# Optimization experiments

Measured on AMD Instinct MI355X. Metric: run time of the kernel, lower is better.

Reference implementation:

```python
import jax, jax.numpy as jnp
import numpy as np

NUM_INPUTS = 256
L1, L2 = 256, 128
NUM_ACTIONS = 17
NUM_EXPERTS = 4
GATE_H = 32
BATCH = 131072


def setup_inputs() -> dict:
    key = jax.random.key(0)
    ks = jax.random.split(key, 16)
    s = 0.05
    return {
        "x": jax.random.normal(ks[0], (BATCH, NUM_INPUTS), jnp.float32),
        # stacked expert weights [E, in, out]
        "W1": jax.random.normal(ks[1], (NUM_EXPERTS, NUM_INPUTS, L1), jnp.float32) * s,
        "b1": jax.random.normal(ks[2], (NUM_EXPERTS, L1), jnp.float32) * s,
        "W2": jax.random.normal(ks[3], (NUM_EXPERTS, L1, L2), jnp.float32) * s,
        "b2": jax.random.normal(ks[4], (NUM_EXPERTS, L2), jnp.float32) * s,
        "Wmu": jax.random.normal(ks[5], (NUM_EXPERTS, L2, NUM_ACTIONS), jnp.float32) * s,
        "bmu": jax.random.normal(ks[6], (NUM_EXPERTS, NUM_ACTIONS), jnp.float32) * s,
        # gate (BlendingModule) params
        "gW1": jax.random.normal(ks[7], (NUM_INPUTS, GATE_H), jnp.float32) * s,
        "gb1": jax.random.normal(ks[8], (GATE_H,), jnp.float32) * s,
        "gW2": jax.random.normal(ks[9], (GATE_H, GATE_H), jnp.float32) * s,
        "gb2": jax.random.normal(ks[10], (GATE_H,), jnp.float32) * s,
        "gWo": jax.random.normal(ks[11], (GATE_H, NUM_EXPERTS), jnp.float32) * s,
        "gbo": jax.random.normal(ks[12], (NUM_EXPERTS,), jnp.float32) * s,
    }


def _gate(x, gW1, gb1, gW2, gb2, gWo, gbo):
    h = jax.nn.elu(x @ gW1 + gb1)
    h = jax.nn.elu(h @ gW2 + gb2)
    return jax.nn.softmax(h @ gWo + gbo, axis=1)  # [B, E]


def reference(x, W1, b1, W2, b2, Wmu, bmu, gW1, gb1, gW2, gb2, gWo, gbo):
    coeffs = _gate(x, gW1, gb1, gW2, gb2, gWo, gbo)  # [B, E]
    # layer 1: gate-weighted sum of 4 expert GEMMs, then ReLU
    h = jnp.einsum("bi,eio->beo", x, W1) + b1[None]          # [B, E, L1]
    h = jax.nn.relu(jnp.einsum("be,beo->bo", coeffs, h))     # [B, L1]
    # layer 2
    h = jnp.einsum("bi,eio->beo", h, W2) + b2[None]          # [B, E, L2]
    h = jax.nn.relu(jnp.einsum("be,beo->bo", coeffs, h))     # [B, L2]
    # output head: weighted sum, no activation
    mu = jnp.einsum("bi,eio->beo", h, Wmu) + bmu[None]       # [B, E, A]
    mu = jnp.einsum("be,beo->bo", coeffs, mu)                # [B, A]
    return mu
```

## Files before the change

### kernel.cpp

```cpp
#include <hip/hip_runtime.h>


typedef _Float16 half8 __attribute__((ext_vector_type(8)));
typedef _Float16 half4v __attribute__((ext_vector_type(4)));
typedef float floatx4 __attribute__((ext_vector_type(4)));

#define MFMA16(a, b, c) __builtin_amdgcn_mfma_f32_16x16x32_f16(a, b, c, 0, 0, 0)
#define WAIT_VM(N) asm volatile("s_waitcnt vmcnt(" #N ")" ::: "memory")
#define WAIT_LGKM0 asm volatile("s_waitcnt lgkmcnt(0)" ::: "memory")

__device__ __forceinline__ void barrier_mem() {
  asm volatile("" ::: "memory");
  __builtin_amdgcn_s_barrier();
  asm volatile("" ::: "memory");
}

__device__ __forceinline__ half8 splat8(_Float16 v) {
  half8 r = {v, v, v, v, v, v, v, v};
  return r;
}

__device__ __forceinline__ half8 make_cfrag(half4v c) {
  half8 r = {c[0], c[1], c[2], c[3], (_Float16)0, (_Float16)0, (_Float16)0, (_Float16)0};
  return r;
}

__device__ __forceinline__ void load_lds16(const _Float16* g, _Float16* s) {
  __builtin_amdgcn_global_load_lds((__attribute__((address_space(1))) void*)(g),
                                   (__attribute__((address_space(3))) void*)(s), 16, 0, 0);
}

enum {
  W1P = 0,
  W2P = 262144,
  WMUP = 393216,
  GW1P = 409600,
  GW2P = 417792,
  GWOP = 418816,
  B1P = 419328,
  B2P = 427520,
  BMUP = 431616,
  GBIASP = 432640,
  WS_TOTAL = 433152
};

__global__ __launch_bounds__(256) void prep_kernel(
    const float* __restrict__ W1, const float* __restrict__ W2,
    const float* __restrict__ Wmu, const float* __restrict__ gW1,
    const float* __restrict__ gW2, const float* __restrict__ gWo,
    const float* __restrict__ b1, const float* __restrict__ b2,
    const float* __restrict__ bmu, const float* __restrict__ gb1,
    const float* __restrict__ gb2, const float* __restrict__ gbo,
    _Float16* __restrict__ ws) {
  int p = blockIdx.x * 256 + threadIdx.x;
  if (p >= WS_TOTAL) return;
  float v = 0.f;
  if (p < W2P) {
    int t = p >> 13, r = p & 8191;
    int ct = r >> 9, l = (r >> 3) & 63, j = r & 7;
    int o = ct * 16 + (l & 15), krel = ((l >> 4) << 3) + j;
    int t8 = t >> 2, e = t & 3;
    v = W1[(e * 256 + t8 * 32 + krel) * 256 + o];
  } else if (p < WMUP) {
    int q = p - W2P, t = q >> 12, r = q & 4095;
    int ct = r >> 9, l = (r >> 3) & 63, j = r & 7;
    int o = ct * 16 + (l & 15), krel = ((l >> 4) << 3) + j;
    int t8 = t >> 2, e = t & 3;
    v = W2[(e * 256 + t8 * 32 + krel) * 128 + o];
  } else if (p < GW1P) {
    int q = p - WMUP, t = q >> 10, r = q & 1023;
    int ct = r >> 9, l = (r >> 3) & 63, j = r & 7;
    int o = ct * 16 + (l & 15), krel = ((l >> 4) << 3) + j;
    int t2 = t >> 2, e = t & 3;
    v = (o < 17) ? Wmu[(e * 128 + t2 * 32 + krel) * 17 + o] : 0.f;
  } else if (p < GW2P) {
    int q = p - GW1P, ks = q >> 10, r = q & 1023;
    int ct = r >> 9, l = (r >> 3) & 63, j = r & 7;
    int o = ct * 16 + (l & 15), krel = ((l >> 4) << 3) + j;
    v = gW1[(ks * 32 + krel) * 32 + o];
  } else if (p < GWOP) {
    int q = p - GW2P;
    int ct = q >> 9, l = (q >> 3) & 63, j = q & 7;
    int o = ct * 16 + (l & 15), krel = ((l >> 4) << 3) + j;
    v = gW2[krel * 32 + o];
  } else if (p < B1P) {
    int q = p - GWOP;
    int l = (q >> 3) & 63, j = q & 7;
    int o = l & 15, krel = ((l >> 4) << 3) + j;
    v = (o < 4) ? gWo[krel * 4 + o] : 0.f;
  } else if (p < B2P) {
    int q = p - B1P;
    int ct = q >> 9, l = (q >> 3) & 63, j = q & 7;
    int o = ct * 16 + (l & 15), krel = ((l >> 4) << 3) + j;
    v = (krel < 4) ? b1[krel * 256 + o] : 0.f;
  } else if (p < BMUP) {
    int q = p - B2P;
    int ct = q >> 9, l = (q >> 3) & 63, j = q & 7;
    int o = ct * 16 + (l & 15), krel = ((l >> 4) << 3) + j;
    v = (krel < 4) ? b2[krel * 128 + o] : 0.f;
  } else if (p < GBIASP) {
    int q = p - BMUP;
    int ct = q >> 9, l = (q >> 3) & 63, j = q & 7;
    int o = ct * 16 + (l & 15), krel = ((l >> 4) << 3) + j;
    v = (krel < 4 && o < 17) ? bmu[krel * 17 + o] : 0.f;
  } else {
    int q = p - GBIASP;
    v = (q < 32) ? gb1[q] : (q < 64) ? gb2[q - 32] : (q < 68) ? gbo[q - 64] : 0.f;
  }
  ws[p] = (_Float16)v;
}

enum {
  STG = 16384,
  GW2L = STG + 8192,
  GWOL = STG + 9216,
  GBL = STG + 9728,
  SCR1 = STG + 10240,
  SCR2 = STG + 12288,
  COEF = STG + 14336,
  LDS_HW = 40960
};
static_assert(LDS_HW * 2 == 81920, "LDS must be exactly 80KB");

__global__ __launch_bounds__(512, 2) void actor_kernel(
    const float* __restrict__ x, const _Float16* __restrict__ ws,
    float* __restrict__ out) {
  __shared__ __align__(16) _Float16 lds[LDS_HW];
  const int tid = threadIdx.x;
  const int l = tid & 63;
  const int w = tid >> 6;
  const int l15 = l & 15;
  const int g8 = (l >> 4) << 3;
  const long rowbase = (long)blockIdx.x * 64;
  const floatx4 z4 = {0.f, 0.f, 0.f, 0.f};

  {
    const float* xp = x + rowbase * 256 + w * 32 + g8;
#pragma unroll
    for (int rt = 0; rt < 4; ++rt) {
      const float* rr = xp + (rt * 16 + l15) * 256;
      float4 v0 = *(const float4*)rr;
      float4 v1 = *(const float4*)(rr + 4);
      half8 h = {(_Float16)v0.x, (_Float16)v0.y, (_Float16)v0.z, (_Float16)v0.w,
                 (_Float16)v1.x, (_Float16)v1.y, (_Float16)v1.z, (_Float16)v1.w};
      *(half8*)(&lds[w * 2048 + rt * 512 + l * 8]) = h;
    }
  }
  for (int c = w; c < 20; c += 8) {
    const _Float16* src;
    _Float16* dst;
    if (c < 16) { src = ws + GW1P + c * 512; dst = lds + STG + c * 512; }
    else if (c < 18) { src = ws + GW2P + (c - 16) * 512; dst = lds + GW2L + (c - 16) * 512; }
    else if (c == 18) { src = ws + GWOP; dst = lds + GWOL; }
    else { src = ws + GBIASP; dst = lds + GBL; }
    load_lds16(src + l * 8, dst);
  }
  load_lds16(ws + B1P + w * 512 + l * 8, lds + STG + 16384 + w * 512);
  load_lds16(ws + B1P + (w + 8) * 512 + l * 8, lds + STG + 16384 + (w + 8) * 512);
  WAIT_LGKM0;
  WAIT_VM(2);
  barrier_mem();

  const int grt = w & 3, gct = w >> 2;
  {
    floatx4 ga = z4;
#pragma unroll
    for (int ks = 0; ks < 8; ++ks) {
      half8 a = *(const half8*)(&lds[ks * 2048 + grt * 512 + l * 8]);
      half8 b = *(const half8*)(&lds[STG + ks * 1024 + gct * 512 + l * 8]);
      ga = MFMA16(a, b, ga);
    }
    const int col = gct * 16 + l15;
    const float bias = (float)lds[GBL + col];
    const int hi4 = ((col >> 3) & 3) << 4, jj = col & 7;
#pragma unroll
    for (int rg = 0; rg < 4; ++rg) {
      float v = ga[rg] + bias;
      v = v > 0.f ? v : (__expf(v) - 1.f);
      lds[SCR1 + grt * 512 + ((4 * (l >> 4) + rg) | hi4) * 8 + jj] = (_Float16)v;
    }
  }
  WAIT_LGKM0;
  barrier_mem();

  {
    half8 a = *(const half8*)(&lds[SCR1 + grt * 512 + l * 8]);
    half8 b = *(const half8*)(&lds[GW2L + gct * 512 + l * 8]);
    floatx4 g2 = MFMA16(a, b, z4);
    const int col = gct * 16 + l15;
    const float bias = (float)lds[GBL + 32 + col];
    const int hi4 = ((col >> 3) & 3) << 4, jj = col & 7;
#pragma unroll
    for (int rg = 0; rg < 4; ++rg) {
      float v = g2[rg] + bias;
      v = v > 0.f ? v : (__expf(v) - 1.f);
      lds[SCR2 + grt * 512 + ((4 * (l >> 4) + rg) | hi4) * 8 + jj] = (_Float16)v;
    }
  }
  WAIT_LGKM0;
  barrier_mem();

  if (gct == 0) {
    half8 a = *(const half8*)(&lds[SCR2 + grt * 512 + l * 8]);
    half8 bo = *(const half8*)(&lds[GWOL + l * 8]);
    floatx4 lg = MFMA16(a, bo, z4);
    const float bze = (l15 < 4) ? (float)lds[GBL + 64 + l15] : 0.f;
#pragma unroll
    for (int rg = 0; rg < 4; ++rg) {
      float v = lg[rg] + bze;
      float m = fmaxf(v, __shfl_xor(v, 1));
      m = fmaxf(m, __shfl_xor(m, 2));
      float eo = __expf(v - m);
      float sden = eo + __shfl_xor(eo, 1);
      sden += __shfl_xor(sden, 2);
      if (l15 < 4)
        lds[COEF + (grt * 16 + 4 * (l >> 4) + rg) * 4 + l15] = (_Float16)(eo / sden);
    }
  }
  WAIT_LGKM0;
  barrier_mem();

  half4v c4[4];
#pragma unroll
  for (int rt = 0; rt < 4; ++rt)
    c4[rt] = *(const half4v*)(&lds[COEF + (rt * 16 + l15) * 4]);
  load_lds16(ws + W1P + w * 512 + l * 8, lds + STG + w * 512);
  load_lds16(ws + W1P + (w + 8) * 512 + l * 8, lds + STG + (w + 8) * 512);
  WAIT_VM(2);
  WAIT_LGKM0;
  barrier_mem();

  floatx4 acc[4][2];
  {
    load_lds16(ws + W1P + 8192 + w * 512 + l * 8, lds + STG + 8192 + w * 512);
    load_lds16(ws + W1P + 8192 + (w + 8) * 512 + l * 8, lds + STG + 8192 + (w + 8) * 512);
    half8 b0 = *(const half8*)(&lds[STG + 16384 + w * 1024 + l * 8]);
    half8 b1v = *(const half8*)(&lds[STG + 16384 + w * 1024 + 512 + l * 8]);
#pragma unroll
    for (int rt = 0; rt < 4; ++rt) {
      half8 cf = make_cfrag(c4[rt]);
      acc[rt][0] = MFMA16(cf, b0, z4);
      acc[rt][1] = MFMA16(cf, b1v, z4);
    }
    WAIT_VM(2);
    barrier_mem();
  }

  half8 af[4];
  int rs = 0;
#pragma unroll 1
  for (int t8 = 0; t8 < 8; ++t8) {
#pragma unroll
    for (int e = 0; e < 4; ++e) {
      const int T = t8 * 4 + e + 1;
      if (T <= 30) {
        const int is3 = (rs >= 1) ? rs - 1 : 2;
        const _Float16* src = ws + W1P + (T + 1) * 8192 + l * 8;
        _Float16* dst = lds + STG + is3 * 8192;
        load_lds16(src + w * 512, dst + w * 512);
        load_lds16(src + (w + 8) * 512, dst + (w + 8) * 512);
      }
      if (e == 0) {
#pragma unroll
        for (int rt = 0; rt < 4; ++rt)
          af[rt] = *(const half8*)(&lds[t8 * 2048 + rt * 512 + l * 8]);
      }
      half8 b0 = *(const half8*)(&lds[STG + rs * 8192 + w * 1024 + l * 8]);
      half8 b1v = *(const half8*)(&lds[STG + rs * 8192 + w * 1024 + 512 + l * 8]);
#pragma unroll
      for (int rt = 0; rt < 4; ++rt) {
        half8 as = af[rt] * splat8(c4[rt][e]);
        acc[rt][0] = MFMA16(as, b0, acc[rt][0]);
        acc[rt][1] = MFMA16(as, b1v, acc[rt][1]);
      }
      if (T <= 30) { WAIT_VM(2); }
      else if (T == 31) { WAIT_VM(0); }
      barrier_mem();
      rs = (rs >= 2) ? 0 : rs + 1;
    }
  }

#pragma unroll
  for (int rt = 0; rt < 4; ++rt)
#pragma unroll
    for (int ct = 0; ct < 2; ++ct) {
      const int c32 = ct * 16 + l15;
      const int hi4 = ((c32 >> 3) & 3) << 4, jj = c32 & 7;
#pragma unroll
      for (int rg = 0; rg < 4; ++rg) {
        float v = acc[rt][ct][rg];
        v = v > 0.f ? v : 0.f;
        lds[w * 2048 + rt * 512 + ((4 * (l >> 4) + rg) | hi4) * 8 + jj] = (_Float16)v;
      }
    }
  load_lds16(ws + B2P + w * 512 + l * 8, lds + STG + 4 * 4096 + w * 512);
  load_lds16(ws + W2P + 0 * 4096 + w * 512 + l * 8, lds + STG + 5 * 4096 + w * 512);
  load_lds16(ws + W2P + 1 * 4096 + w * 512 + l * 8, lds + STG + 0 * 4096 + w * 512);
  load_lds16(ws + W2P + 2 * 4096 + w * 512 + l * 8, lds + STG + 1 * 4096 + w * 512);
  WAIT_LGKM0;
  WAIT_VM(3);
  barrier_mem();

  floatx4 acc2[4];
  {
    load_lds16(ws + W2P + 3 * 4096 + w * 512 + l * 8, lds + STG + 2 * 4096 + w * 512);
    half8 b0 = *(const half8*)(&lds[STG + 4 * 4096 + w * 512 + l * 8]);
#pragma unroll
    for (int rt = 0; rt < 4; ++rt) {
      half8 cf = make_cfrag(c4[rt]);
      acc2[rt] = MFMA16(cf, b0, z4);
    }
    WAIT_VM(3);
    barrier_mem();
  }

  int rs6 = 5, is6 = 3;
#pragma unroll 1
  for (int t8 = 0; t8 < 8; ++t8) {
#pragma unroll
    for (int e = 0; e < 4; ++e) {
      const int T = t8 * 4 + e + 1;
      if (T <= 28)
        load_lds16(ws + W2P + (T + 3) * 4096 + w * 512 + l * 8,
                   lds + STG + is6 * 4096 + w * 512);
      if (e == 0) {
#pragma unroll
        for (int rt = 0; rt < 4; ++rt)
          af[rt] = *(const half8*)(&lds[t8 * 2048 + rt * 512 + l * 8]);
      }
      half8 b0 = *(const half8*)(&lds[STG + rs6 * 4096 + w * 512 + l * 8]);
#pragma unroll
      for (int rt = 0; rt < 4; ++rt) {
        half8 as = af[rt] * splat8(c4[rt][e]);
        acc2[rt] = MFMA16(as, b0, acc2[rt]);
      }
      if (T <= 28) { WAIT_VM(3); }
      else if (T == 29) { WAIT_VM(2); }
      else if (T == 30) { WAIT_VM(1); }
      else if (T == 31) { WAIT_VM(0); }
      barrier_mem();
      rs6 = (rs6 >= 5) ? 0 : rs6 + 1;
      is6 = (is6 >= 5) ? 0 : is6 + 1;
    }
  }

  {
    const int c32 = ((w & 1) << 4) | l15;
    const int hi4 = ((c32 >> 3) & 3) << 4, jj = c32 & 7;
#pragma unroll
    for (int rt = 0; rt < 4; ++rt)
#pragma unroll
      for (int rg = 0; rg < 4; ++rg) {
        float v = acc2[rt][rg];
        v = v > 0.f ? v : 0.f;
        lds[(w >> 1) * 2048 + rt * 512 + ((4 * (l >> 4) + rg) | hi4) * 8 + jj] = (_Float16)v;
      }
  }
  for (int c = w; c < 34; c += 8) {
    const _Float16* src = (c < 2) ? (ws + BMUP + c * 512) : (ws + WMUP + (c - 2) * 512);
    load_lds16(src + l * 8, lds + STG + c * 512);
  }
  WAIT_LGKM0;
  WAIT_VM(0);
  barrier_mem();

  {
    const int hrt = w & 3, hct = w >> 2;
    half8 cf = make_cfrag(c4[hrt]);
    half8 b = *(const half8*)(&lds[STG + hct * 512 + l * 8]);
    floatx4 hacc = MFMA16(cf, b, z4);
    half8 ah;
#pragma unroll
    for (int t = 0; t < 16; ++t) {
      if ((t & 3) == 0)
        ah = *(const half8*)(&lds[(t >> 2) * 2048 + hrt * 512 + l * 8]);
      half8 as = ah * splat8(c4[hrt][t & 3]);
      half8 bh = *(const half8*)(&lds[STG + (t + 1) * 1024 + hct * 512 + l * 8]);
      hacc = MFMA16(as, bh, hacc);
    }
    const int col = hct * 16 + l15;
    if (col < 17) {
#pragma unroll
      for (int rg = 0; rg < 4; ++rg)
        out[(rowbase + hrt * 16 + 4 * (l >> 4) + rg) * 17 + col] = hacc[rg];
    }
  }
}

extern "C" void kernel_launch(void* const* d_in, const int* in_sizes, int n_in,
                              void* d_out, int out_size, void* d_ws, size_t ws_size,
                              hipStream_t stream) {
  const float* x = (const float*)d_in[0];
  const float* W1 = (const float*)d_in[1];
  const float* b1 = (const float*)d_in[2];
  const float* W2 = (const float*)d_in[3];
  const float* b2 = (const float*)d_in[4];
  const float* Wmu = (const float*)d_in[5];
  const float* bmu = (const float*)d_in[6];
  const float* gW1 = (const float*)d_in[7];
  const float* gb1 = (const float*)d_in[8];
  const float* gW2 = (const float*)d_in[9];
  const float* gb2 = (const float*)d_in[10];
  const float* gWo = (const float*)d_in[11];
  const float* gbo = (const float*)d_in[12];
  float* out = (float*)d_out;
  _Float16* ws = (_Float16*)d_ws;

  prep_kernel<<<(WS_TOTAL + 255) / 256, 256, 0, stream>>>(
      W1, W2, Wmu, gW1, gW2, gWo, b1, b2, bmu, gb1, gb2, gbo, ws);
  actor_kernel<<<2048, 512, 0, stream>>>(x, ws, out);
}
```

Before: 372.5 us.

## Shrink LDS to 64KB with shallower weight pipelines for four blocks per CU

Result: slower. 975.4 us (+161.8%).

```diff
diff --git a/kernel.cpp b/kernel.cpp
--- a/kernel.cpp
+++ b/kernel.cpp
@@ -118,11 +118,11 @@
   SCR1 = STG + 10240,
   SCR2 = STG + 12288,
   COEF = STG + 14336,
-  LDS_HW = 40960
+  LDS_HW = 32768
 };
-static_assert(LDS_HW * 2 == 81920, "LDS must be exactly 80KB");
-
-__global__ __launch_bounds__(512, 2) void actor_kernel(
+static_assert(LDS_HW * 2 == 65536, "LDS must be exactly 64KB");
+
+__global__ __launch_bounds__(512, 4) void actor_kernel(
     const float* __restrict__ x, const _Float16* __restrict__ ws,
     float* __restrict__ out) {
   __shared__ __align__(16) _Float16 lds[LDS_HW];
@@ -155,10 +155,8 @@
     else { src = ws + GBIASP; dst = lds + GBL; }
     load_lds16(src + l * 8, dst);
   }
-  load_lds16(ws + B1P + w * 512 + l * 8, lds + STG + 16384 + w * 512);
-  load_lds16(ws + B1P + (w + 8) * 512 + l * 8, lds + STG + 16384 + (w + 8) * 512);
-  WAIT_LGKM0;
-  WAIT_VM(2);
+  WAIT_LGKM0;
+  WAIT_VM(0);
   barrier_mem();
 
   const int grt = w & 3, gct = w >> 2;
@@ -224,39 +222,39 @@
 #pragma unroll
   for (int rt = 0; rt < 4; ++rt)
     c4[rt] = *(const half4v*)(&lds[COEF + (rt * 16 + l15) * 4]);
-  load_lds16(ws + W1P + w * 512 + l * 8, lds + STG + w * 512);
-  load_lds16(ws + W1P + (w + 8) * 512 + l * 8, lds + STG + (w + 8) * 512);
+  WAIT_LGKM0;
+  barrier_mem();
+
+  load_lds16(ws + B1P + w * 512 + l * 8, lds + STG + w * 512);
+  load_lds16(ws + B1P + (w + 8) * 512 + l * 8, lds + STG + (w + 8) * 512);
+  load_lds16(ws + W1P + w * 512 + l * 8, lds + STG + 8192 + w * 512);
+  load_lds16(ws + W1P + (w + 8) * 512 + l * 8, lds + STG + 8192 + (w + 8) * 512);
   WAIT_VM(2);
-  WAIT_LGKM0;
   barrier_mem();
 
   floatx4 acc[4][2];
   {
-    load_lds16(ws + W1P + 8192 + w * 512 + l * 8, lds + STG + 8192 + w * 512);
-    load_lds16(ws + W1P + 8192 + (w + 8) * 512 + l * 8, lds + STG + 8192 + (w + 8) * 512);
-    half8 b0 = *(const half8*)(&lds[STG + 16384 + w * 1024 + l * 8]);
-    half8 b1v = *(const half8*)(&lds[STG + 16384 + w * 1024 + 512 + l * 8]);
+    half8 b0 = *(const half8*)(&lds[STG + w * 1024 + l * 8]);
+    half8 b1v = *(const half8*)(&lds[STG + w * 1024 + 512 + l * 8]);
 #pragma unroll
     for (int rt = 0; rt < 4; ++rt) {
       half8 cf = make_cfrag(c4[rt]);
       acc[rt][0] = MFMA16(cf, b0, z4);
       acc[rt][1] = MFMA16(cf, b1v, z4);
     }
-    WAIT_VM(2);
+    WAIT_VM(0);
     barrier_mem();
   }
 
   half8 af[4];
-  int rs = 0;
 #pragma unroll 1
   for (int t8 = 0; t8 < 8; ++t8) {
 #pragma unroll
     for (int e = 0; e < 4; ++e) {
-      const int T = t8 * 4 + e + 1;
-      if (T <= 30) {
-        const int is3 = (rs >= 1) ? rs - 1 : 2;
-        const _Float16* src = ws + W1P + (T + 1) * 8192 + l * 8;
-        _Float16* dst = lds + STG + is3 * 8192;
+      const int p = t8 * 4 + e + 1;
+      if (p <= 31) {
+        const _Float16* src = ws + W1P + p * 8192 + l * 8;
+        _Float16* dst = lds + STG + ((p + 1) & 1) * 8192;
         load_lds16(src + w * 512, dst + w * 512);
         load_lds16(src + (w + 8) * 512, dst + (w + 8) * 512);
       }
@@ -265,18 +263,17 @@
         for (int rt = 0; rt < 4; ++rt)
           af[rt] = *(const half8*)(&lds[t8 * 2048 + rt * 512 + l * 8]);
       }
-      half8 b0 = *(const half8*)(&lds[STG + rs * 8192 + w * 1024 + l * 8]);
-      half8 b1v = *(const half8*)(&lds[STG + rs * 8192 + w * 1024 + 512 + l * 8]);
+      const int ss = STG + (p & 1) * 8192;
+      half8 b0 = *(const half8*)(&lds[ss + w * 1024 + l * 8]);
+      half8 b1v = *(const half8*)(&lds[ss + w * 1024 + 512 + l * 8]);
 #pragma unroll
       for (int rt = 0; rt < 4; ++rt) {
         half8 as = af[rt] * splat8(c4[rt][e]);
         acc[rt][0] = MFMA16(as, b0, acc[rt][0]);
         acc[rt][1] = MFMA16(as, b1v, acc[rt][1]);
       }
-      if (T <= 30) { WAIT_VM(2); }
-      else if (T == 31) { WAIT_VM(0); }
+      WAIT_VM(0);
       barrier_mem();
-      rs = (rs >= 2) ? 0 : rs + 1;
     }
   }
 
@@ -293,54 +290,47 @@
         lds[w * 2048 + rt * 512 + ((4 * (l >> 4) + rg) | hi4) * 8 + jj] = (_Float16)v;
       }
     }
-  load_lds16(ws + B2P + w * 512 + l * 8, lds + STG + 4 * 4096 + w * 512);
-  load_lds16(ws + W2P + 0 * 4096 + w * 512 + l * 8, lds + STG + 5 * 4096 + w * 512);
-  load_lds16(ws + W2P + 1 * 4096 + w * 512 + l * 8, lds + STG + 0 * 4096 + w * 512);
-  load_lds16(ws + W2P + 2 * 4096 + w * 512 + l * 8, lds + STG + 1 * 4096 + w * 512);
-  WAIT_LGKM0;
-  WAIT_VM(3);
+  load_lds16(ws + B2P + w * 512 + l * 8, lds + STG + w * 512);
+  load_lds16(ws + W2P + w * 512 + l * 8, lds + STG + 4096 + w * 512);
+  WAIT_LGKM0;
+  WAIT_VM(1);
   barrier_mem();
 
   floatx4 acc2[4];
   {
-    load_lds16(ws + W2P + 3 * 4096 + w * 512 + l * 8, lds + STG + 2 * 4096 + w * 512);
-    half8 b0 = *(const half8*)(&lds[STG + 4 * 4096 + w * 512 + l * 8]);
+    load_lds16(ws + W2P + 4096 + w * 512 + l * 8, lds + STG + 2 * 4096 + w * 512);
+    half8 b0 = *(const half8*)(&lds[STG + w * 512 + l * 8]);
 #pragma unroll
     for (int rt = 0; rt < 4; ++rt) {
       half8 cf = make_cfrag(c4[rt]);
       acc2[rt] = MFMA16(cf, b0, z4);
     }
-    WAIT_VM(3);
+    WAIT_VM(1);
     barrier_mem();
   }
 
-  int rs6 = 5, is6 = 3;
 #pragma unroll 1
   for (int t8 = 0; t8 < 8; ++t8) {
 #pragma unroll
     for (int e = 0; e < 4; ++e) {
-      const int T = t8 * 4 + e + 1;
-      if (T <= 28)
-        load_lds16(ws + W2P + (T + 3) * 4096 + w * 512 + l * 8,
-                   lds + STG + is6 * 4096 + w * 512);
+      const int p = t8 * 4 + e + 1;
+      if (p <= 30)
+        load_lds16(ws + W2P + (p + 1) * 4096 + w * 512 + l * 8,
+                   lds + STG + ((p + 2) & 3) * 4096 + w * 512);
       if (e == 0) {
 #pragma unroll
         for (int rt = 0; rt < 4; ++rt)
           af[rt] = *(const half8*)(&lds[t8 * 2048 + rt * 512 + l * 8]);
       }
-      half8 b0 = *(const half8*)(&lds[STG + rs6 * 4096 + w * 512 + l * 8]);
+      half8 b0 = *(const half8*)(&lds[STG + (p & 3) * 4096 + w * 512 + l * 8]);
 #pragma unroll
       for (int rt = 0; rt < 4; ++rt) {
         half8 as = af[rt] * splat8(c4[rt][e]);
         acc2[rt] = MFMA16(as, b0, acc2[rt]);
       }
-      if (T <= 28) { WAIT_VM(3); }
-      else if (T == 29) { WAIT_VM(2); }
-      else if (T == 30) { WAIT_VM(1); }
-      else if (T == 31) { WAIT_VM(0); }
+      if (p <= 30) { WAIT_VM(1); }
+      else if (p == 31) { WAIT_VM(0); }
       barrier_mem();
-      rs6 = (rs6 >= 5) ? 0 : rs6 + 1;
-      is6 = (is6 >= 5) ? 0 : is6 + 1;
     }
   }
 
@@ -356,10 +346,9 @@
         lds[(w >> 1) * 2048 + rt * 512 + ((4 * (l >> 4) + rg) | hi4) * 8 + jj] = (_Float16)v;
       }
   }
-  for (int c = w; c < 34; c += 8) {
-    const _Float16* src = (c < 2) ? (ws + BMUP + c * 512) : (ws + WMUP + (c - 2) * 512);
-    load_lds16(src + l * 8, lds + STG + c * 512);
-  }
+  for (int c = w; c < 32; c += 8)
+    load_lds16(ws + WMUP + c * 512 + l * 8, lds + STG + c * 512);
+  if (w < 2) load_lds16(ws + BMUP + w * 512 + l * 8, lds + 8192 + w * 512);
   WAIT_LGKM0;
   WAIT_VM(0);
   barrier_mem();
@@ -367,7 +356,7 @@
   {
     const int hrt = w & 3, hct = w >> 2;
     half8 cf = make_cfrag(c4[hrt]);
-    half8 b = *(const half8*)(&lds[STG + hct * 512 + l * 8]);
+    half8 b = *(const half8*)(&lds[8192 + hct * 512 + l * 8]);
     floatx4 hacc = MFMA16(cf, b, z4);
     half8 ah;
 #pragma unroll
@@ -375,7 +364,7 @@
       if ((t & 3) == 0)
         ah = *(const half8*)(&lds[(t >> 2) * 2048 + hrt * 512 + l * 8]);
       half8 as = ah * splat8(c4[hrt][t & 3]);
-      half8 bh = *(const half8*)(&lds[STG + (t + 1) * 1024 + hct * 512 + l * 8]);
+      half8 bh = *(const half8*)(&lds[STG + t * 1024 + hct * 512 + l * 8]);
       hacc = MFMA16(as, bh, hacc);
     }
     const int col = hct * 16 + l15;
```
